# Kernel optimization log

Measured on AMD Instinct MI355X. Metric: run time of the kernel, lower is better.

Reference implementation:

```python
import jax, jax.numpy as jnp
import numpy as np

L, H, C, HS, V, BS = 4, 4, 1024, 256, 32000, 1024  # layers, heads, n_embd, head_size, vocab, block_size
B, T = 4, 1024
EPS = 1e-5

def _ln(x, g, b):
    mu = jnp.mean(x, axis=-1, keepdims=True)
    var = jnp.mean((x - mu) ** 2, axis=-1, keepdims=True)
    return (x - mu) / jnp.sqrt(var + EPS) * g + b

def setup_inputs() -> dict:
    key = jax.random.key(0)
    ks = iter(jax.random.split(key, 32))
    s = 0.02
    inp = {
        'idx': jax.random.randint(next(ks), (B, T), 0, V),
        'tok_emb': jax.random.normal(next(ks), (V, C), jnp.float32) * s,
        'pos_emb': jax.random.normal(next(ks), (BS, C), jnp.float32) * s,
        'wq': jax.random.normal(next(ks), (L, H, C, HS), jnp.float32) * s,
        'wk': jax.random.normal(next(ks), (L, H, C, HS), jnp.float32) * s,
        'wv': jax.random.normal(next(ks), (L, H, C, HS), jnp.float32) * s,
        'proj_w': jax.random.normal(next(ks), (L, C, C), jnp.float32) * s,
        'proj_b': jnp.zeros((L, C), jnp.float32),
        'ln1_g': jnp.ones((L, C), jnp.float32),
        'ln1_b': jnp.zeros((L, C), jnp.float32),
        'ln2_g': jnp.ones((L, C), jnp.float32),
        'ln2_b': jnp.zeros((L, C), jnp.float32),
        'ff_w1': jax.random.normal(next(ks), (L, C, 4 * C), jnp.float32) * s,
        'ff_b1': jnp.zeros((L, 4 * C), jnp.float32),
        'ff_w2': jax.random.normal(next(ks), (L, 4 * C, C), jnp.float32) * s,
        'ff_b2': jnp.zeros((L, C), jnp.float32),
        'lnf_g': jnp.ones((C,), jnp.float32),
        'lnf_b': jnp.zeros((C,), jnp.float32),
        'head_w': jax.random.normal(next(ks), (C, V), jnp.float32) * s,
        'head_b': jnp.zeros((V,), jnp.float32),
    }
    return inp

def reference(idx, tok_emb, pos_emb, wq, wk, wv, proj_w, proj_b, ln1_g, ln1_b,
              ln2_g, ln2_b, ff_w1, ff_b1, ff_w2, ff_b2, lnf_g, lnf_b, head_w, head_b):
    b, t = idx.shape
    x = tok_emb[idx] + pos_emb[:t]  # (B,T,C)
    causal = jnp.tril(jnp.ones((t, t), bool))
    inv_sqrt_c = np.float32(1.0 / np.sqrt(C))  # NOTE: original scales by sqrt(n_embd), not head_size
    for l in range(L):
        xn = _ln(x, ln1_g[l], ln1_b[l])
        q = jnp.einsum('btc,hcd->bhtd', xn, wq[l])
        k = jnp.einsum('bsc,hcd->bhsd', xn, wk[l])
        v = jnp.einsum('bsc,hcd->bhsd', xn, wv[l])
        scores = jnp.einsum('bhtd,bhsd->bhts', q, k)
        scores = jnp.where(causal, scores, -jnp.inf) * inv_sqrt_c
        # original: F.softmax(xdot, dim=1) on (B,T,T) -> normalize over the QUERY axis
        alpha = jax.nn.softmax(scores, axis=2)
        y = jnp.einsum('bhts,bhsd->bhtd', alpha, v)
        y = y.transpose(0, 2, 1, 3).reshape(b, t, C)  # concat heads
        x = x + y @ proj_w[l] + proj_b[l]
        xn2 = _ln(x, ln2_g[l], ln2_b[l])
        h = jax.nn.relu(xn2 @ ff_w1[l] + ff_b1[l])
        x = x + h @ ff_w2[l] + ff_b2[l]
    x = _ln(x, lnf_g, lnf_b)
    logits = x @ head_w + head_b  # (B,T,V)
    return logits
```

## Files before the change

### kernel.cpp

```cpp
#include <hip/hip_runtime.h>


#define C_  1024
#define T_  1024
#define HS_ 256
#define H_  4
#define L_  4
#define V_  32000
#define B_  4
#define M_  4096

typedef __attribute__((ext_vector_type(8))) short  bfx8;
typedef __attribute__((ext_vector_type(4))) float  fx4;
typedef __attribute__((ext_vector_type(4))) unsigned short usx4;
typedef __attribute__((ext_vector_type(8))) unsigned short usx8;

__device__ __forceinline__ unsigned short f2bf(float f) {
  unsigned int u = __builtin_bit_cast(unsigned int, f);
  u += 0x7fffu + ((u >> 16) & 1u);
  return (unsigned short)(u >> 16);
}
__device__ __forceinline__ float bf2f(unsigned short u) {
  return __builtin_bit_cast(float, ((unsigned int)u) << 16);
}

__device__ __forceinline__ void gload16(const unsigned short* g, unsigned short* l) {
  __builtin_amdgcn_global_load_lds(
      (const __attribute__((address_space(1))) unsigned int*)g,
      (__attribute__((address_space(3))) unsigned int*)l, 16, 0, 0);
}

template<int BIAS, int RES, int RELU, int OUTBF, int TRI>
__global__ __launch_bounds__(256, 2) void gemm_bf16(
    const unsigned short* __restrict__ A, const unsigned short* __restrict__ Bm,
    const float* __restrict__ bias, const float* __restrict__ res,
    void* __restrict__ out,
    int M, int N, int K, int lda, int ldb, int ldc,
    long sA, long sB, long sC1, long sC2, int zShift, long rowOuter)
{
  __shared__ unsigned short As[128 * 32];
  __shared__ unsigned short Bs[128 * 32];
  const int z = blockIdx.z;
  A  += (long)z * sA;
  Bm += (long)z * sB;
  const long outOff = ((long)(z >> zShift)) * sC1 + (long)(z & ((1 << zShift) - 1)) * sC2;
  const int m0 = blockIdx.x * 128, n0 = blockIdx.y * 128;
  if (TRI) K = min(K, m0 + 128);
  const int tid = threadIdx.x;
  const int lane = tid & 63, wave = tid >> 6;
  const int wm = (wave >> 1) * 64, wn = (wave & 1) * 64;
  const int fr = lane & 15, kb = lane >> 4;
  const int sr = lane >> 2;
  const int csw = (((lane & 3) ^ ((lane >> 3) & 3)) << 3);
  const int aco = ((kb ^ ((lane >> 1) & 3)) << 3);

  fx4 acc[4][4] = {};

  for (int k0 = 0; k0 < K; k0 += 32) {
    #pragma unroll
    for (int i = 0; i < 2; ++i) {
      const int c = wave * 2 + i;
      gload16(A  + (long)(m0 + c * 16 + sr) * lda + k0 + csw, &As[c * 512]);
      gload16(Bm + (long)(n0 + c * 16 + sr) * ldb + k0 + csw, &Bs[c * 512]);
    }
    __syncthreads();
    bfx8 af[4], bf[4];
    #pragma unroll
    for (int i = 0; i < 4; ++i)
      af[i] = *reinterpret_cast<const bfx8*>(&As[(wm + i * 16 + fr) * 32 + aco]);
    #pragma unroll
    for (int j = 0; j < 4; ++j)
      bf[j] = *reinterpret_cast<const bfx8*>(&Bs[(wn + j * 16 + fr) * 32 + aco]);
    #pragma unroll
    for (int i = 0; i < 4; ++i)
      #pragma unroll
      for (int j = 0; j < 4; ++j)
        acc[i][j] = __builtin_amdgcn_mfma_f32_16x16x32_bf16(af[i], bf[j], acc[i][j], 0, 0, 0);
    __syncthreads();
  }

  const float* resp = res;
  if (RES) resp += outOff;
  const int rbase = (lane >> 4) * 4;
  #pragma unroll
  for (int j = 0; j < 4; ++j) {
    const int n = n0 + wn + j * 16 + fr;
    float bv = 0.f;
    if (BIAS) bv = bias[n];
    #pragma unroll
    for (int i = 0; i < 4; ++i) {
      #pragma unroll
      for (int r = 0; r < 4; ++r) {
        const int m = m0 + wm + i * 16 + rbase + r;
        const long off = outOff + ((long)(m >> 10)) * rowOuter + (long)(m & 1023) * ldc + n;
        float val = acc[i][j][r] + bv;
        if (RELU) val = fmaxf(val, 0.f);
        if (RES) val += resp[((long)(m >> 10)) * rowOuter + (long)(m & 1023) * ldc + n];
        if (OUTBF) ((unsigned short*)out)[off] = f2bf(val);
        else       ((float*)out)[off] = val;
      }
    }
  }
}

#define BAR() __builtin_amdgcn_s_barrier()
#define LGKM() { asm volatile("s_waitcnt lgkmcnt(0)" ::: "memory"); \
                 __builtin_amdgcn_sched_barrier(0); }
#define VM8()  asm volatile("s_waitcnt vmcnt(8)" ::: "memory")
#define STA(tau, kh) { const int tc = (tau) < NT ? (tau) : NT - 1; \
  const unsigned short* src = A + (long)(m0 + wave * 16 + srow) * lda + tc * 64 + (kh) * 32 + csw; \
  unsigned short* d = &S[(((tau) & 1) * 2 + (kh)) * 8192 + wave * 512]; \
  gload16(src, d); gload16(src + (long)128 * lda, d + 4096); }
#define STB(tau, kh) { const int tc = (tau) < NT ? (tau) : NT - 1; \
  const unsigned short* src = Bm + (long)(n0 + wave * 16 + srow) * ldb + tc * 64 + (kh) * 32 + csw; \
  unsigned short* d = &S[32768 + (((tau) & 1) * 2 + (kh)) * 8192 + wave * 512]; \
  gload16(src, d); gload16(src + (long)128 * ldb, d + 4096); }
#define RDA8(dst, par, kh) { _Pragma("unroll") for (int i = 0; i < 8; ++i) \
  dst[i] = *reinterpret_cast<const bfx8*>(&S[((par)*2+(kh))*8192 + (wr*128 + i*16 + fr)*32 + aco]); }
#define RDB(dst, par, kh) { _Pragma("unroll") for (int j = 0; j < 4; ++j) \
  dst[j] = *reinterpret_cast<const bfx8*>(&S[32768 + ((par)*2+(kh))*8192 + (wc*64 + j*16 + fr)*32 + aco]); }
#define MM32(afx, bfx) { __builtin_amdgcn_s_setprio(1); \
  _Pragma("unroll") for (int i = 0; i < 8; ++i) { _Pragma("unroll") for (int j = 0; j < 4; ++j) \
    acc[i][j] = __builtin_amdgcn_mfma_f32_16x16x32_bf16(afx[i], bfx[j], acc[i][j], 0, 0, 0); } \
  __builtin_amdgcn_s_setprio(0); }

template<int BIAS, int RELU, int OUTBF, int EPI, int TRI>
__global__ __launch_bounds__(512, 2) void gemm256(
    const unsigned short* __restrict__ A, const unsigned short* __restrict__ Bm,
    const float* __restrict__ bias, void* __restrict__ out,
    int K, int lda, int ldb, int ldc, long sA, long sB, long sC1)
{
  __shared__ unsigned short S[65536];
  if (TRI && blockIdx.y < blockIdx.x) return;
  const int z = blockIdx.z;
  A  += (long)z * sA;
  Bm += (long)z * sB;
  const long outOff = (long)z * sC1;
  const int m0 = blockIdx.x * 256, n0 = blockIdx.y * 256;
  const int tid = threadIdx.x;
  const int lane = tid & 63, wave = tid >> 6;
  const int wr = wave >> 2, wc = wave & 3;
  const int fr = lane & 15, kb = lane >> 4;
  const int srow = lane >> 2;
  const int csw = (((lane & 3) ^ (((lane >> 5) & 1) << 1)) << 3);
  const int aco = ((kb ^ (((fr >> 3) & 1) << 1)) << 3);
  const int NT = K >> 6;
  const int NK4 = K >> 7;

  fx4 acc[8][4] = {};
  bfx8 afa[8], afb[8], bfa[4], bfb[4];

  STB(0, 0); STA(0, 0); STB(0, 1); STA(0, 1);
  STB(1, 0); STA(1, 0); STB(1, 1); STA(1, 1);
  VM8(); BAR();
  RDA8(afa, 0, 0); RDB(bfa, 0, 0);
  LGKM(); BAR();

  for (int t = 0; t < NK4; ++t) {
    const int u = 2 * t;
    STA(u + 2, 0); STB(u + 2, 0); RDA8(afb, 0, 1); RDB(bfb, 0, 1);
    MM32(afa, bfa); LGKM(); VM8(); BAR();
    STA(u + 2, 1); STB(u + 2, 1); RDA8(afa, 1, 0); RDB(bfa, 1, 0);
    MM32(afb, bfb); LGKM(); VM8(); BAR();
    STA(u + 3, 0); STB(u + 3, 0); RDA8(afb, 1, 1); RDB(bfb, 1, 1);
    MM32(afa, bfa); LGKM(); VM8(); BAR();
    STA(u + 3, 1); STB(u + 3, 1); RDA8(afa, 0, 0); RDB(bfa, 0, 0);
    MM32(afb, bfb); LGKM(); VM8(); BAR();
  }
  asm volatile("s_waitcnt vmcnt(0)" ::: "memory");
  BAR();

  const int rbase = (lane >> 4) * 4;
  unsigned short* dst1 = nullptr;
  if (EPI == 1) {
    const int sel = n0 >> 10, h = (n0 >> 8) & 3;
    const int bq = m0 >> 10, tq0 = m0 & 1023;
    dst1 = (unsigned short*)out + ((long)sel * B_ + bq) * H_ * T_ * HS_
         + (long)h * T_ * HS_ + (long)tq0 * HS_;
  }
  float* lf = (float*)S;
  #pragma unroll
  for (int jh = 0; jh < 2; ++jh) {
    #pragma unroll
    for (int jj = 0; jj < 2; ++jj)
      #pragma unroll
      for (int i = 0; i < 8; ++i)
        #pragma unroll
        for (int r = 0; r < 4; ++r) {
          const int row = i * 16 + rbase + r;
          const int cw = (jj * 16 + fr) ^ ((row & 7) << 2);
          lf[wave * 4096 + row * 32 + cw] = acc[i][jh * 2 + jj][r];
        }
    #pragma unroll
    for (int rs = 0; rs < 16; ++rs) {
      const int row = rs * 8 + (lane >> 3);
      const int c0 = (lane & 7) * 4;
      const int cw = c0 ^ ((row & 7) << 2);
      fx4 val = *reinterpret_cast<const fx4*>(&lf[wave * 4096 + row * 32 + cw]);
      const int nl = wc * 64 + jh * 32 + c0;
      if (BIAS) {
        const float4 bb = *reinterpret_cast<const float4*>(bias + n0 + nl);
        val[0] += bb.x; val[1] += bb.y; val[2] += bb.z; val[3] += bb.w;
      }
      if (RELU) {
        val[0] = fmaxf(val[0], 0.f); val[1] = fmaxf(val[1], 0.f);
        val[2] = fmaxf(val[2], 0.f); val[3] = fmaxf(val[3], 0.f);
      }
      if (EPI == 1) {
        const long off = (long)(wr * 128 + row) * HS_ + nl;
        usx4 o = { f2bf(val[0]), f2bf(val[1]), f2bf(val[2]), f2bf(val[3]) };
        *reinterpret_cast<usx4*>(dst1 + off) = o;
      } else {
        const long off = outOff + (long)(m0 + wr * 128 + row) * ldc + n0 + nl;
        if (OUTBF) {
          usx4 o = { f2bf(val[0]), f2bf(val[1]), f2bf(val[2]), f2bf(val[3]) };
          *reinterpret_cast<usx4*>((unsigned short*)out + off) = o;
        } else {
          __builtin_nontemporal_store(val, reinterpret_cast<fx4*>((float*)out + off));
        }
      }
    }
    __builtin_amdgcn_sched_barrier(0);
  }
}

template<typename TIN>
__global__ __launch_bounds__(256) void transpose_k(const TIN* __restrict__ src,
    unsigned short* __restrict__ dst, int R, int Cc, int zShiftT, long sOuter) {
  __shared__ float ts[64][65];
  const long zb = blockIdx.z;
  src += zb * (long)R * Cc;
  dst += (zb >> zShiftT) * sOuter + (zb & ((1 << zShiftT) - 1)) * ((long)R * Cc);
  const int r0 = blockIdx.y * 64, c0 = blockIdx.x * 64;
  const int tr = threadIdx.x >> 4;
  const int tc = (threadIdx.x & 15) * 4;
  #pragma unroll
  for (int it = 0; it < 4; ++it) {
    const int r = tr + it * 16;
    float4 v;
    if constexpr (sizeof(TIN) == 4) {
      v = *reinterpret_cast<const float4*>(src + (long)(r0 + r) * Cc + c0 + tc);
    } else {
      usx4 u = *reinterpret_cast<const usx4*>(src + (long)(r0 + r) * Cc + c0 + tc);
      v.x = bf2f(u[0]); v.y = bf2f(u[1]); v.z = bf2f(u[2]); v.w = bf2f(u[3]);
    }
    ts[r][tc + 0] = v.x; ts[r][tc + 1] = v.y; ts[r][tc + 2] = v.z; ts[r][tc + 3] = v.w;
  }
  __syncthreads();
  #pragma unroll
  for (int it = 0; it < 4; ++it) {
    const int cj = tr + it * 16;
    usx4 o = { f2bf(ts[tc + 0][cj]), f2bf(ts[tc + 1][cj]),
               f2bf(ts[tc + 2][cj]), f2bf(ts[tc + 3][cj]) };
    *reinterpret_cast<usx4*>(dst + (long)(c0 + cj) * R + r0 + tc) = o;
  }
}

__global__ __launch_bounds__(256) void embed_k(const int* __restrict__ idx,
                                               const float* __restrict__ tok,
                                               const float* __restrict__ pos,
                                               float* __restrict__ x) {
  const int row = blockIdx.x;
  const int t = row & (T_ - 1);
  const int id = idx[row];
  const int c = threadIdx.x * 4;
  const float4 a = *reinterpret_cast<const float4*>(tok + (long)id * C_ + c);
  const float4 p = *reinterpret_cast<const float4*>(pos + (long)t * C_ + c);
  float4 ov = { a.x + p.x, a.y + p.y, a.z + p.z, a.w + p.w };
  *reinterpret_cast<float4*>(x + (long)row * C_ + c) = ov;
}

__global__ __launch_bounds__(256) void ln_k(const float* __restrict__ x,
                                            const float* __restrict__ g,
                                            const float* __restrict__ b,
                                            unsigned short* __restrict__ o) {
  __shared__ float red[8];
  const int row = blockIdx.x;
  const int c = threadIdx.x * 4;
  const float4 v = *reinterpret_cast<const float4*>(x + (long)row * C_ + c);
  float s1 = v.x + v.y + v.z + v.w;
  float s2 = v.x * v.x + v.y * v.y + v.z * v.z + v.w * v.w;
  #pragma unroll
  for (int off = 32; off; off >>= 1) {
    s1 += __shfl_xor(s1, off, 64);
    s2 += __shfl_xor(s2, off, 64);
  }
  const int lane = threadIdx.x & 63, w = threadIdx.x >> 6;
  if (lane == 0) { red[w] = s1; red[4 + w] = s2; }
  __syncthreads();
  s1 = red[0] + red[1] + red[2] + red[3];
  s2 = red[4] + red[5] + red[6] + red[7];
  const float mu = s1 * (1.f / C_);
  float var = s2 * (1.f / C_) - mu * mu;
  var = fmaxf(var, 0.f);
  const float inv = rsqrtf(var + 1e-5f);
  const float4 gg = *reinterpret_cast<const float4*>(g + c);
  const float4 bb = *reinterpret_cast<const float4*>(b + c);
  usx4 ov;
  ov[0] = f2bf((v.x - mu) * inv * gg.x + bb.x);
  ov[1] = f2bf((v.y - mu) * inv * gg.y + bb.y);
  ov[2] = f2bf((v.z - mu) * inv * gg.z + bb.z);
  ov[3] = f2bf((v.w - mu) * inv * gg.w + bb.w);
  *reinterpret_cast<usx4*>(o + (long)row * C_ + c) = ov;
}

__global__ __launch_bounds__(256) void colsmT_k(const unsigned short* __restrict__ sc,
                                                unsigned short* __restrict__ alpha) {
  __shared__ float invs[64];
  __shared__ float tile[64][65];
  const int z = blockIdx.z;
  const int s0 = blockIdx.x * 64;
  const int r = threadIdx.x >> 2;
  const int tq = threadIdx.x & 3;
  const int s = s0 + r;
  const unsigned short* p = sc + (long)z * T_ * T_ + (long)s * T_ + tq * 256;
  const float scale = 0.03125f;

  float zsum = 0.f;
  for (int i = 0; i < 32; ++i) {
    const usx8 u = *reinterpret_cast<const usx8*>(p + i * 8);
    #pragma unroll
    for (int j = 0; j < 8; ++j) {
      const int t = tq * 256 + i * 8 + j;
      if (t >= s) zsum += __expf(bf2f(u[j]) * scale);
    }
  }
  zsum += __shfl_xor(zsum, 1, 64);
  zsum += __shfl_xor(zsum, 2, 64);
  if (tq == 0) invs[r] = 1.f / zsum;
  __syncthreads();
  const float inv = invs[r];

  const unsigned short* prow = sc + (long)z * T_ * T_ + (long)s * T_;
  unsigned short* ob = alpha + (long)z * T_ * T_ + s0;
  const int wrow = threadIdx.x >> 2;
  const int seg  = threadIdx.x & 3;
  for (int tc = 0; tc < 16; ++tc) {
    #pragma unroll
    for (int half = 0; half < 2; ++half) {
      const int tb = tc * 64 + tq * 16 + half * 8;
      const usx8 u = *reinterpret_cast<const usx8*>(prow + tb);
      #pragma unroll
      for (int j = 0; j < 8; ++j) {
        const int t = tb + j;
        const float a = (t >= s) ? __expf(bf2f(u[j]) * scale) * inv : 0.f;
        tile[tq * 16 + half * 8 + j][r] = a;
      }
    }
    __syncthreads();
    usx8 o0, o1;
    #pragma unroll
    for (int k = 0; k < 8; ++k) o0[k] = f2bf(tile[wrow][seg * 16 + k]);
    #pragma unroll
    for (int k = 0; k < 8; ++k) o1[k] = f2bf(tile[wrow][seg * 16 + 8 + k]);
    unsigned short* od = ob + (long)(tc * 64 + wrow) * T_ + seg * 16;
    *reinterpret_cast<usx8*>(od) = o0;
    *reinterpret_cast<usx8*>(od + 8) = o1;
    __syncthreads();
  }
}

extern "C" void kernel_launch(void* const* d_in, const int* in_sizes, int n_in,
                              void* d_out, int out_size, void* d_ws, size_t ws_size,
                              hipStream_t stream) {
  const int*   idx    = (const int*)d_in[0];
  const float* tok    = (const float*)d_in[1];
  const float* pos    = (const float*)d_in[2];
  const float* wq     = (const float*)d_in[3];
  const float* wk     = (const float*)d_in[4];
  const float* wv     = (const float*)d_in[5];
  const float* proj_w = (const float*)d_in[6];
  const float* proj_b = (const float*)d_in[7];
  const float* ln1_g  = (const float*)d_in[8];
  const float* ln1_b  = (const float*)d_in[9];
  const float* ln2_g  = (const float*)d_in[10];
  const float* ln2_b  = (const float*)d_in[11];
  const float* ff_w1  = (const float*)d_in[12];
  const float* ff_b1  = (const float*)d_in[13];
  const float* ff_w2  = (const float*)d_in[14];
  const float* ff_b2  = (const float*)d_in[15];
  const float* lnf_g  = (const float*)d_in[16];
  const float* lnf_b  = (const float*)d_in[17];
  const float* head_w = (const float*)d_in[18];
  const float* head_b = (const float*)d_in[19];
  float* outp = (float*)d_out;

  typedef unsigned short us;
  char* w = (char*)d_ws;
  float* x    = (float*)(w + 0);
  us* xn      = (us*)(w + 16777216);
  us* qkv     = (us*)(w + 25165824);
  us* kptr    = qkv + 4194304;
  us* vptr    = qkv + 8388608;
  us* vT      = (us*)(w + 50331648);
  us* yc      = (us*)(w + 58720256);
  us* sc      = (us*)(w + 67108864);
  us* headT   = (us*)(w + 67108864);
  us* alpha   = (us*)(w + 100663296);
  us* hidden  = (us*)(w + 134217728);
  us* wqkvT   = (us*)(w + 167772160);
  us* projT   = (us*)(w + 192937984);
  us* ff1T    = (us*)(w + 201326592);
  us* ff2T    = (us*)(w + 234881024);
  if (ws_size < (size_t)268435456) return;

  const long HHC = (long)H_ * HS_ * C_;
  transpose_k<float><<<dim3(HS_/64, C_/64, L_*H_), 256, 0, stream>>>(wq, wqkvT,           C_, HS_, 2, 3*HHC);
  transpose_k<float><<<dim3(HS_/64, C_/64, L_*H_), 256, 0, stream>>>(wk, wqkvT + HHC,     C_, HS_, 2, 3*HHC);
  transpose_k<float><<<dim3(HS_/64, C_/64, L_*H_), 256, 0, stream>>>(wv, wqkvT + 2*HHC,   C_, HS_, 2, 3*HHC);
  transpose_k<float><<<dim3(C_/64, C_/64, L_), 256, 0, stream>>>(proj_w, projT, C_, C_, 0, (long)C_*C_);
  transpose_k<float><<<dim3(4*C_/64, C_/64, L_), 256, 0, stream>>>(ff_w1, ff1T, C_, 4*C_, 0, (long)C_*4*C_);
  transpose_k<float><<<dim3(C_/64, 4*C_/64, L_), 256, 0, stream>>>(ff_w2, ff2T, 4*C_, C_, 0, (long)4*C_*C_);

  embed_k<<<M_, 256, 0, stream>>>(idx, tok, pos, x);

  for (int l = 0; l < L_; ++l) {
    ln_k<<<M_, 256, 0, stream>>>(x, ln1_g + l * C_, ln1_b + l * C_, xn);

    dim3 gqkv(M_/256, 3*C_/256, 1);
    gemm256<0,0,1,1,0><<<gqkv, 512, 0, stream>>>(xn, wqkvT + l * 3 * HHC, nullptr, qkv,
        C_, C_, C_, 0, 0, 0, 0);

    dim3 gs(T_/256, T_/256, B_*H_);
    gemm256<0,0,1,0,1><<<gs, 512, 0, stream>>>(kptr, qkv, nullptr, sc,
        HS_, HS_, HS_, T_, (long)T_*HS_, (long)T_*HS_, (long)T_*T_);

    colsmT_k<<<dim3(T_/64, 1, B_*H_), 256, 0, stream>>>(sc, alpha);

    transpose_k<us><<<dim3(HS_/64, T_/64, B_*H_), 256, 0, stream>>>(vptr, vT, T_, HS_, 0, (long)T_*HS_);

    dim3 gp(T_/128, HS_/128, B_*H_);
    gemm_bf16<0,0,0,1,1><<<gp, 256, 0, stream>>>(alpha, vT, nullptr, nullptr, yc,
        T_, HS_, T_, T_, T_, C_, (long)T_*T_, (long)HS_*T_, (long)T_*C_, HS_, 2, (long)T_*C_);

    dim3 gj(M_/128, C_/128, 1);
    gemm_bf16<1,1,0,0,0><<<gj, 256, 0, stream>>>(yc, projT + (long)l*C_*C_, proj_b + l*C_, x, x,
        M_, C_, C_, C_, C_, C_, 0, 0, 0, 0, 0, (long)T_*C_);

    ln_k<<<M_, 256, 0, stream>>>(x, ln2_g + l * C_, ln2_b + l * C_, xn);

    dim3 g1(M_/256, 4*C_/256, 1);
    gemm256<1,1,1,0,0><<<g1, 512, 0, stream>>>(xn, ff1T + (long)l*4*C_*C_, ff_b1 + (long)l*4*C_,
        hidden, C_, C_, C_, 4*C_, 0, 0, 0);

    dim3 g2(M_/128, C_/128, 1);
    gemm_bf16<1,1,0,0,0><<<g2, 256, 0, stream>>>(hidden, ff2T + (long)l*C_*4*C_, ff_b2 + l*C_, x, x,
        M_, C_, 4*C_, 4*C_, 4*C_, C_, 0, 0, 0, 0, 0, (long)T_*C_);
  }

  ln_k<<<M_, 256, 0, stream>>>(x, lnf_g, lnf_b, xn);

  transpose_k<float><<<dim3(V_/64, C_/64, 1), 256, 0, stream>>>(head_w, headT, C_, V_, 0, (long)C_*V_);

  dim3 gh(M_/256, V_/256, 1);
  gemm256<1,0,0,0,0><<<gh, 512, 0, stream>>>(xn, headT, head_b, outp,
      C_, C_, C_, V_, 0, 0, 0);
}
```

Baseline: 1.850 ms.

## Split GEMM main loop into half-tile MFMA phases with finer LDS prefetch

The 256x256 bf16 GEMM main loop is restructured so each k-half is processed in two row-halves of A fragments (4 instead of 8 per read). LDS reads, global-to-LDS loads and MFMA batches are interleaved at a finer grain, with twice as many barriers. The goal is to cut register pressure from the A fragment buffers and overlap LDS reads with smaller MFMA groups more evenly. In exchange, the doubled barrier count adds synchronisation overhead, and the hazard ordering on the double-buffered LDS must stay correct.

```diff
diff --git a/kernel.cpp b/kernel.cpp
--- a/kernel.cpp
+++ b/kernel.cpp
@@ -115,13 +115,13 @@
   const unsigned short* src = Bm + (long)(n0 + wave * 16 + srow) * ldb + tc * 64 + (kh) * 32 + csw; \
   unsigned short* d = &S[32768 + (((tau) & 1) * 2 + (kh)) * 8192 + wave * 512]; \
   gload16(src, d); gload16(src + (long)128 * ldb, d + 4096); }
-#define RDA8(dst, par, kh) { _Pragma("unroll") for (int i = 0; i < 8; ++i) \
-  dst[i] = *reinterpret_cast<const bfx8*>(&S[((par)*2+(kh))*8192 + (wr*128 + i*16 + fr)*32 + aco]); }
+#define RDA(dst, par, kh, rh) { _Pragma("unroll") for (int i = 0; i < 4; ++i) \
+  dst[i] = *reinterpret_cast<const bfx8*>(&S[((par)*2+(kh))*8192 + (wr*128 + (rh)*64 + i*16 + fr)*32 + aco]); }
 #define RDB(dst, par, kh) { _Pragma("unroll") for (int j = 0; j < 4; ++j) \
   dst[j] = *reinterpret_cast<const bfx8*>(&S[32768 + ((par)*2+(kh))*8192 + (wc*64 + j*16 + fr)*32 + aco]); }
-#define MM32(afx, bfx) { __builtin_amdgcn_s_setprio(1); \
-  _Pragma("unroll") for (int i = 0; i < 8; ++i) { _Pragma("unroll") for (int j = 0; j < 4; ++j) \
-    acc[i][j] = __builtin_amdgcn_mfma_f32_16x16x32_bf16(afx[i], bfx[j], acc[i][j], 0, 0, 0); } \
+#define MM(rh, afx, bfx) { __builtin_amdgcn_s_setprio(1); \
+  _Pragma("unroll") for (int i = 0; i < 4; ++i) { _Pragma("unroll") for (int j = 0; j < 4; ++j) \
+    acc[(rh)*4+i][j] = __builtin_amdgcn_mfma_f32_16x16x32_bf16(afx[i], bfx[j], acc[(rh)*4+i][j], 0, 0, 0); } \
   __builtin_amdgcn_s_setprio(0); }
 
 template<int BIAS, int RELU, int OUTBF, int EPI, int TRI>
@@ -145,27 +145,29 @@
   const int csw = (((lane & 3) ^ (((lane >> 5) & 1) << 1)) << 3);
   const int aco = ((kb ^ (((fr >> 3) & 1) << 1)) << 3);
   const int NT = K >> 6;
-  const int NK4 = K >> 7;
+  const int NI = NT >> 1;
 
   fx4 acc[8][4] = {};
-  bfx8 afa[8], afb[8], bfa[4], bfb[4];
+  bfx8 afa[4], afb[4], bf0[4], bf1[4];
 
   STB(0, 0); STA(0, 0); STB(0, 1); STA(0, 1);
   STB(1, 0); STA(1, 0); STB(1, 1); STA(1, 1);
-  VM8(); BAR();
-  RDA8(afa, 0, 0); RDB(bfa, 0, 0);
-  LGKM(); BAR();
-
-  for (int t = 0; t < NK4; ++t) {
+  VM8();
+  BAR();
+  RDA(afa, 0, 0, 0); RDB(bf1, 0, 0);
+  LGKM();
+  BAR();
+
+  for (int t = 0; t < NI; ++t) {
     const int u = 2 * t;
-    STA(u + 2, 0); STB(u + 2, 0); RDA8(afb, 0, 1); RDB(bfb, 0, 1);
-    MM32(afa, bfa); LGKM(); VM8(); BAR();
-    STA(u + 2, 1); STB(u + 2, 1); RDA8(afa, 1, 0); RDB(bfa, 1, 0);
-    MM32(afb, bfb); LGKM(); VM8(); BAR();
-    STA(u + 3, 0); STB(u + 3, 0); RDA8(afb, 1, 1); RDB(bfb, 1, 1);
-    MM32(afa, bfa); LGKM(); VM8(); BAR();
-    STA(u + 3, 1); STB(u + 3, 1); RDA8(afa, 0, 0); RDB(bfa, 0, 0);
-    MM32(afb, bfb); LGKM(); VM8(); BAR();
+    STB(u + 2, 0); RDA(afb, 0, 0, 1);                 MM(0, afa, bf1); LGKM(); BAR();
+    STA(u + 2, 0); RDA(afa, 0, 1, 0); RDB(bf0, 0, 1); MM(1, afb, bf1); LGKM(); VM8(); BAR();
+    STB(u + 2, 1); RDA(afb, 0, 1, 1);                 MM(0, afa, bf0); LGKM(); BAR();
+    STA(u + 2, 1); RDA(afa, 1, 0, 0); RDB(bf1, 1, 0); MM(1, afb, bf0); LGKM(); VM8(); BAR();
+    STB(u + 3, 0); RDA(afb, 1, 0, 1);                 MM(0, afa, bf1); LGKM(); BAR();
+    STA(u + 3, 0); RDA(afa, 1, 1, 0); RDB(bf0, 1, 1); MM(1, afb, bf1); LGKM(); VM8(); BAR();
+    STB(u + 3, 1); RDA(afb, 1, 1, 1);                 MM(0, afa, bf0); LGKM(); BAR();
+    STA(u + 3, 1); RDA(afa, 0, 0, 0); RDB(bf1, 0, 0); MM(1, afb, bf0); LGKM(); VM8(); BAR();
   }
   asm volatile("s_waitcnt vmcnt(0)" ::: "memory");
   BAR();
```

After: 1.530 ms. 1.21x faster.
